# Performance work log

Hardware: AMD Instinct MI355X
Metric: run time of the kernel (lower is better)

## Reference

```python
import jax, jax.numpy as jnp
import numpy as np

N = 100000   # nodes
D = 256      # in_dim == out_dim
R = 4        # num_rel
T = 150000   # triangles per relation
H = 2        # nheads (num_rel >= 2)
DH = D // H
EPS = 1e-5


def _layernorm(x, g, b):
    m = jnp.mean(x, axis=-1, keepdims=True)
    v = jnp.mean((x - m) ** 2, axis=-1, keepdims=True)
    return (x - m) * jax.lax.rsqrt(v + EPS) * g + b


def setup_inputs() -> dict:
    key = jax.random.key(0)
    ks = jax.random.split(key, 24)
    s = 1.0 / np.sqrt(D)
    f32 = jnp.float32
    inp = {}
    inp["x"] = jax.random.normal(ks[0], (N, D), f32)
    inp["triangles"] = jax.random.randint(ks[1], (R, 3, T), 0, N)
    inp["edge_index"] = jax.random.randint(ks[2], (R, 2, 8), 0, N)
    inp["node_W"] = jax.random.normal(ks[3], (R, D, D), f32) * s
    inp["tri_W"] = jax.random.normal(ks[4], (R, D, D), f32) * s
    inp["res_W"] = jax.random.normal(ks[5], (D, D), f32) * s
    inp["gate_W"] = jax.random.normal(ks[6], (D, 2 * D), f32) * (1.0 / np.sqrt(2 * D))
    inp["gate_b"] = jnp.zeros((D,), f32)
    inp["in_W"] = jax.random.normal(ks[7], (3 * D, D), f32) * s
    inp["in_b"] = jnp.zeros((3 * D,), f32)
    inp["out_W"] = jax.random.normal(ks[8], (D, D), f32) * s
    inp["out_b"] = jnp.zeros((D,), f32)
    inp["ln1_g"] = jnp.ones((D,), f32)
    inp["ln1_b"] = jnp.zeros((D,), f32)
    inp["lin1_W"] = jax.random.normal(ks[9], (2 * D, D), f32) * s
    inp["lin1_b"] = jnp.zeros((2 * D,), f32)
    inp["lin2_W"] = jax.random.normal(ks[10], (D, 2 * D), f32) * (1.0 / np.sqrt(2 * D))
    inp["lin2_b"] = jnp.zeros((D,), f32)
    inp["ln2_g"] = jnp.ones((D,), f32)
    inp["ln2_b"] = jnp.zeros((D,), f32)
    return inp


def reference(x, triangles, edge_index, node_W, tri_W, res_W, gate_W, gate_b,
              in_W, in_b, out_W, out_b, ln1_g, ln1_b,
              lin1_W, lin1_b, lin2_W, lin2_b, ln2_g, ln2_b):
    del edge_index  # unused by the original forward
    x_res = x @ res_W.T  # [N, D]
    hs = []
    for r in range(R):  # small fixed relation count
        tri = triangles[r]                                 # [3, T]
        tri_feat = (x[tri] @ node_W[r].T).mean(axis=0)     # [T, D]
        tri_msg = tri_feat @ tri_W[r].T                    # [T, D]
        idx = tri.T.reshape(-1)                            # [3T], triangle-major
        rep = jnp.repeat(tri_msg, 3, axis=0)               # [3T, D]
        ssum = jax.ops.segment_sum(rep, idx, num_segments=N)
        cnt = jax.ops.segment_sum(jnp.ones((3 * T,), x.dtype), idx, num_segments=N)
        node_msg = ssum / jnp.maximum(cnt, 1.0)[:, None]   # scatter_mean
        u = jax.nn.elu(node_msg)                           # dropout = identity (eval)
        a = jax.nn.sigmoid(jnp.concatenate([x, u], axis=1) @ gate_W.T + gate_b)
        hs.append(jnp.tanh(u) * a + x_res * (1.0 - a))
    src = jnp.stack(hs, axis=0)                            # [R, N, D] (seq, batch, d)

    # single post-norm TransformerEncoderLayer over the relation axis
    qkv = src @ in_W.T + in_b                              # [R, N, 3D]
    q, k, v = jnp.split(qkv, 3, axis=-1)
    q = q.reshape(R, N, H, DH)
    k = k.reshape(R, N, H, DH)
    v = v.reshape(R, N, H, DH)
    scores = jnp.einsum('qnhd,knhd->nhqk', q, k) / np.sqrt(DH)
    attn = jax.nn.softmax(scores, axis=-1)
    o = jnp.einsum('nhqk,knhd->qnhd', attn, v).reshape(R, N, D)
    o = o @ out_W.T + out_b
    x1 = _layernorm(src + o, ln1_g, ln1_b)
    ff = jax.nn.gelu(x1 @ lin1_W.T + lin1_b, approximate=False) @ lin2_W.T + lin2_b
    x2 = _layernorm(x1 + ff, ln2_g, ln2_b)
    return x2.mean(axis=0)                                 # [N, D]
```

## Files before the change

kernel.cpp:

```cpp
#include <hip/hip_runtime.h>


#define NNODES 100000
#define NPAD   100096
#define DIM    256
#define NREL   4
#define NTRI   150000

typedef unsigned short ushortT;
typedef __attribute__((ext_vector_type(8)))  short   short8;
typedef __attribute__((ext_vector_type(4)))  float   floatx4;
typedef __attribute__((ext_vector_type(4)))  unsigned short ushort4v;

__device__ __forceinline__ float bf2f(ushortT u) {
    union { unsigned int i; float f; } c; c.i = ((unsigned int)u) << 16; return c.f;
}
__device__ __forceinline__ ushortT f2bf(float f) {
    union { float f; unsigned int i; } c; c.f = f;
    unsigned int x = c.i;
    x += 0x7fffu + ((x >> 16) & 1u);
    return (ushortT)(x >> 16);
}


__global__ void cvt_f32_bf16(const float* __restrict__ in, ushortT* __restrict__ out, int n4) {
    int i = blockIdx.x * blockDim.x + threadIdx.x;
    int stride = gridDim.x * blockDim.x;
    for (; i < n4; i += stride) {
        float4 v = ((const float4*)in)[i];
        ushort4v o; o.x = f2bf(v.x); o.y = f2bf(v.y); o.z = f2bf(v.z); o.w = f2bf(v.w);
        ((ushort4v*)out)[i] = o;
    }
}

__global__ void wcomb_kernel(const float* __restrict__ nodeW, const float* __restrict__ triW,
                             ushortT* __restrict__ wcomb) {
    int idx = blockIdx.x * 256 + threadIdx.x;
    int r = idx >> 16, o = (idx >> 8) & 255, k = idx & 255;
    const float* tw = triW  + ((size_t)r << 16) + o * 256;
    const float* nw = nodeW + ((size_t)r << 16) + k;
    float s = 0.f;
    #pragma unroll 8
    for (int j = 0; j < 256; ++j) s += tw[j] * nw[(size_t)j * 256];
    wcomb[idx] = f2bf(s);
}

__global__ void pack_xg(const float* __restrict__ resW, const float* __restrict__ gateW,
                        ushortT* __restrict__ o) {
    int idx = blockIdx.x * 256 + threadIdx.x;
    int r = idx >> 8, k = idx & 255;
    float v = (r < 256) ? resW[r * 256 + k] : gateW[(size_t)(r - 256) * 512 + k];
    o[idx] = f2bf(v);
}

__global__ void pack_wvo(const float* __restrict__ outW, const float* __restrict__ inW,
                         ushortT* __restrict__ o) {
    int idx = blockIdx.x * 256 + threadIdx.x;
    int r = idx >> 8, k = idx & 255;
    int orow = r & 255, d0 = (r >> 8) * 128;
    float s = 0.f;
    #pragma unroll 8
    for (int j = 0; j < 128; ++j)
        s += outW[orow * 256 + d0 + j] * inW[(size_t)(512 + d0 + j) * 256 + k];
    o[idx] = f2bf(s);
}

__global__ void calc_bvo(const float* __restrict__ outW, const float* __restrict__ in_b,
                         float* __restrict__ bvo) {
    int c = blockIdx.x * 256 + threadIdx.x;
    int orow = c & 255, d0 = (c >> 8) * 128;
    float s = 0.f;
    #pragma unroll 8
    for (int j = 0; j < 128; ++j) s += outW[orow * 256 + d0 + j] * in_b[512 + d0 + j];
    bvo[c] = s;
}


__global__ void k_count(const int* __restrict__ tri3, int* __restrict__ cnt, int n3) {
    int i = blockIdx.x * 256 + threadIdx.x;
    if (i < n3) atomicAdd(&cnt[tri3[i]], 1);
}

__global__ void k_scan1(const int* __restrict__ cnt, int* __restrict__ ptr,
                        int* __restrict__ bsum, int n) {
    __shared__ int s[256];
    int i = blockIdx.x * 256 + threadIdx.x;
    int v = (i < n) ? cnt[i] : 0;
    s[threadIdx.x] = v; __syncthreads();
    for (int off = 1; off < 256; off <<= 1) {
        int t = (threadIdx.x >= off) ? s[threadIdx.x - off] : 0;
        __syncthreads();
        s[threadIdx.x] += t;
        __syncthreads();
    }
    if (i < n) ptr[i] = s[threadIdx.x] - v;
    if (threadIdx.x == 255) bsum[blockIdx.x] = s[255];
}

__global__ void k_scan2(const int* __restrict__ bsum, int* __restrict__ bpre, int nb) {
    int lane = threadIdx.x & 63;
    int run = 0;
    for (int c = 0; c < nb; c += 64) {
        int idx = c + lane;
        int v = (idx < nb) ? bsum[idx] : 0;
        int incl = v;
        #pragma unroll
        for (int off = 1; off < 64; off <<= 1) {
            int t = __shfl_up(incl, off, 64);
            if (lane >= off) incl += t;
        }
        if (idx < nb) bpre[idx] = run + incl - v;
        run += __shfl(incl, 63, 64);
    }
}

__global__ void k_scan3(const int* __restrict__ bpre, int* __restrict__ ptr,
                        int* __restrict__ cursor, int n) {
    int i = blockIdx.x * 256 + threadIdx.x;
    if (i < n) { int p = ptr[i] + bpre[blockIdx.x]; ptr[i] = p; cursor[i] = p; }
}

__global__ void k_fill(const int* __restrict__ tri3, int* __restrict__ cursor,
                       int* __restrict__ adj, int n3, int T) {
    int i = blockIdx.x * 256 + threadIdx.x;
    if (i >= n3) return;
    int node = tri3[i];
    int t = i; if (t >= 2 * T) t -= 2 * T; else if (t >= T) t -= T;
    int pos = atomicAdd(&cursor[node], 1);
    adj[pos] = t;
}

__global__ __launch_bounds__(256)
void k_meanx(const int* __restrict__ tri, const ushortT* __restrict__ xb,
             ushortT* __restrict__ mx, int T) {
    int t = blockIdx.x * 4 + (threadIdx.x >> 6);
    if (t >= T) return;
    int lane = threadIdx.x & 63;
    int a = tri[t], b = tri[T + t], c = tri[2 * T + t];
    ushort4v va = *(const ushort4v*)(xb + (size_t)a * DIM + lane * 4);
    ushort4v vb = *(const ushort4v*)(xb + (size_t)b * DIM + lane * 4);
    ushort4v vc = *(const ushort4v*)(xb + (size_t)c * DIM + lane * 4);
    ushort4v o;
    o.x = f2bf((bf2f(va.x) + bf2f(vb.x) + bf2f(vc.x)) * (1.0f / 3.0f));
    o.y = f2bf((bf2f(va.y) + bf2f(vb.y) + bf2f(vc.y)) * (1.0f / 3.0f));
    o.z = f2bf((bf2f(va.z) + bf2f(vb.z) + bf2f(vc.z)) * (1.0f / 3.0f));
    o.w = f2bf((bf2f(va.w) + bf2f(vb.w) + bf2f(vc.w)) * (1.0f / 3.0f));
    *(ushort4v*)(mx + (size_t)t * DIM + lane * 4) = o;
}

__global__ __launch_bounds__(256)
void k_gather(const int* __restrict__ ptr, const int* __restrict__ cnt,
              const int* __restrict__ adj, const ushortT* __restrict__ mx,
              ushortT* __restrict__ accb, int n) {
    int node = blockIdx.x * 4 + (threadIdx.x >> 6);
    if (node >= n) return;
    int lane = threadIdx.x & 63;
    int st = ptr[node], c = cnt[node];
    float a0 = 0.f, a1 = 0.f, a2 = 0.f, a3 = 0.f;
    for (int j = 0; j < c; ++j) {
        int t = adj[st + j];
        ushort4v v = *(const ushort4v*)(mx + (size_t)t * DIM + lane * 4);
        a0 += bf2f(v.x); a1 += bf2f(v.y); a2 += bf2f(v.z); a3 += bf2f(v.w);
    }
    float inv = 1.0f / fmaxf((float)c, 1.0f);
    ushort4v o; o.x = f2bf(a0 * inv); o.y = f2bf(a1 * inv);
    o.z = f2bf(a2 * inv); o.w = f2bf(a3 * inv);
    *(ushort4v*)(accb + (size_t)node * DIM + lane * 4) = o;
}


#define BK 32

__device__ __forceinline__ void async_cp16(char* lds, const char* glb) {
    __builtin_amdgcn_global_load_lds((const __attribute__((address_space(1))) unsigned int*)glb,
                                     (__attribute__((address_space(3))) unsigned int*)lds,
                                     16, 0, 0);
}

enum { M_BF16 = 0, M_ELU = 1, M_GATE = 2, M_QKV = 3, M_RES = 4, M_GELU = 5 };

template <int MODE>
__global__ __launch_bounds__(256)
void gemm_bt(const ushortT* __restrict__ A, int lda, size_t aStrZ,
             const ushortT* __restrict__ W, int ldw, size_t wStrZ,
             int M, int K,
             ushortT* __restrict__ outB, int ldo, size_t oStrZ,
             const float* __restrict__ bias,
             const ushortT* __restrict__ aux1,
             const ushortT* __restrict__ aux2,
             int auxLd,
             const ushortT* __restrict__ resB,
             size_t resStrZ) {
    const size_t zi = blockIdx.z;
    A += zi * aStrZ; W += zi * wStrZ;
    if (outB) outB += zi * oStrZ;
    if (resB) resB += zi * resStrZ;

    __shared__ __align__(16) ushortT As[2][128 * BK];
    __shared__ __align__(16) ushortT Bs[2][128 * BK];
    const int tid  = threadIdx.x;
    const int wave = tid >> 6, lane = tid & 63;
    const int m0 = blockIdx.y * 128;
    const int n0 = blockIdx.x * 128;
    const int wm = (wave >> 1) * 64, wn = (wave & 1) * 64;

    floatx4 acc[4][4];
    #pragma unroll
    for (int i = 0; i < 4; ++i)
        #pragma unroll
        for (int j = 0; j < 4; ++j) acc[i][j] = (floatx4){0.f, 0.f, 0.f, 0.f};

    const int r4  = tid >> 2;
    const int b16 = (tid & 3) * 16;
    const char* Ab = (const char*)A + ((size_t)(m0 + r4) * lda) * 2 + b16;
    const char* Wb = (const char*)W + ((size_t)(n0 + r4) * ldw) * 2 + b16;

    const int kq = (lane >> 4) * 8;
    const int ra = wm + (lane & 15);
    const int rb = wn + (lane & 15);

    auto stage = [&](int buf, int k0) {
        char* Asl = (char*)As + buf * 8192 + wave * 1024;
        char* Bsl = (char*)Bs + buf * 8192 + wave * 1024;
        async_cp16(Asl,        Ab + k0 * 2);
        async_cp16(Asl + 4096, Ab + k0 * 2 + (size_t)64 * lda * 2);
        async_cp16(Bsl,        Wb + k0 * 2);
        async_cp16(Bsl + 4096, Wb + k0 * 2 + (size_t)64 * ldw * 2);
    };
    auto compute = [&](int buf) {
        short8 af[4], bfr[4];
        #pragma unroll
        for (int i = 0; i < 4; ++i) {
            af[i]  = *(const short8*)(&As[buf][(ra + i * 16) * BK + kq]);
            bfr[i] = *(const short8*)(&Bs[buf][(rb + i * 16) * BK + kq]);
        }
        #pragma unroll
        for (int mi = 0; mi < 4; ++mi)
            #pragma unroll
            for (int ni = 0; ni < 4; ++ni)
                acc[mi][ni] = __builtin_amdgcn_mfma_f32_16x16x32_bf16(af[mi], bfr[ni], acc[mi][ni], 0, 0, 0);
    };

    stage(0, 0);
    __syncthreads();
    int cur = 0;
    for (int k0 = BK; k0 < K; k0 += BK) {
        stage(cur ^ 1, k0);
        compute(cur);
        __syncthreads();
        cur ^= 1;
    }
    compute(cur);

    const int cl = lane & 15, rw = (lane >> 4) * 4;
    #pragma unroll
    for (int mi = 0; mi < 4; ++mi) {
        #pragma unroll
        for (int e = 0; e < 4; ++e) {
            const int m = m0 + wm + mi * 16 + rw + e;
            if (m >= M) continue;
            #pragma unroll
            for (int ni = 0; ni < 4; ++ni) {
                const int col = n0 + wn + ni * 16 + cl;
                float c = acc[mi][ni][e];
                if (MODE == M_BF16) {
                    outB[(size_t)m * ldo + col] = f2bf(c);
                } else if (MODE == M_ELU) {
                    c = c > 0.f ? c : (__expf(c) - 1.0f);
                    outB[(size_t)m * ldo + col] = f2bf(c);
                } else if (MODE == M_GATE) {
                    float g  = bf2f(aux1[(size_t)m * auxLd + col]);
                    float xr = bf2f(aux2[(size_t)m * auxLd + col]);
                    float uv = bf2f(A[(size_t)m * lda + col]);
                    float a  = 1.0f / (1.0f + __expf(-(c + g + bias[col])));
                    float th = 1.0f - 2.0f / (__expf(2.0f * uv) + 1.0f);
                    float h  = th * a + xr * (1.0f - a);
                    outB[(size_t)m * ldo + col] = f2bf(h);
                } else if (MODE == M_QKV) {
                    outB[(size_t)m * ldo + col] = f2bf(c + bias[col]);
                } else if (MODE == M_RES) {
                    outB[(size_t)m * ldo + col] =
                        f2bf(c + bias[col] + bf2f(resB[(size_t)m * 256 + col]));
                } else if (MODE == M_GELU) {
                    float t = c + bias[col];
                    outB[(size_t)m * ldo + col] = f2bf(0.5f * t * (1.0f + erff(t * 0.70710678118f)));
                }
            }
        }
    }
}

__global__ __launch_bounds__(256)
void attn_score(const ushortT* __restrict__ qk, size_t rstride,
                float* __restrict__ Aw, int nvalid) {
    int n = blockIdx.x * 4 + (threadIdx.x >> 6);
    if (n >= nvalid) return;
    int lane = threadIdx.x & 63;
    int head = lane >> 5, hl = lane & 31;
    int d = head * 128 + hl * 4;
    float q[NREL][4], k[NREL][4];
    #pragma unroll
    for (int r = 0; r < NREL; ++r) {
        const ushortT* base = qk + r * rstride + (size_t)n * 512;
        ushort4v qv = *(const ushort4v*)(base + d);
        ushort4v kv = *(const ushort4v*)(base + 256 + d);
        q[r][0] = bf2f(qv.x); q[r][1] = bf2f(qv.y); q[r][2] = bf2f(qv.z); q[r][3] = bf2f(qv.w);
        k[r][0] = bf2f(kv.x); k[r][1] = bf2f(kv.y); k[r][2] = bf2f(kv.z); k[r][3] = bf2f(kv.w);
    }
    float s[NREL][NREL];
    #pragma unroll
    for (int qr = 0; qr < NREL; ++qr)
        #pragma unroll
        for (int kr = 0; kr < NREL; ++kr) {
            float p = q[qr][0] * k[kr][0] + q[qr][1] * k[kr][1] +
                      q[qr][2] * k[kr][2] + q[qr][3] * k[kr][3];
            #pragma unroll
            for (int off = 1; off < 32; off <<= 1) p += __shfl_xor(p, off, 32);
            s[qr][kr] = p * 0.08838834764831845f;
        }
    if (hl < 16) {
        int qr = hl >> 2, kr = hl & 3;
        float mx = fmaxf(fmaxf(s[qr][0], s[qr][1]), fmaxf(s[qr][2], s[qr][3]));
        float e0 = __expf(s[qr][0] - mx), e1 = __expf(s[qr][1] - mx);
        float e2 = __expf(s[qr][2] - mx), e3 = __expf(s[qr][3] - mx);
        float e  = __expf(s[qr][kr] - mx);
        Aw[((size_t)n * 2 + head) * 16 + qr * 4 + kr] = e / (e0 + e1 + e2 + e3);
    }
}

__global__ __launch_bounds__(256)
void attn_combine_ln1(const ushortT* __restrict__ vo4, size_t rstride,
                      const ushortT* __restrict__ h4, size_t hstride,
                      const float* __restrict__ Aw,
                      const float* __restrict__ ob,
                      const float* __restrict__ g, const float* __restrict__ b,
                      ushortT* __restrict__ x1, size_t x1str, int nvalid) {
    int n = blockIdx.x * 4 + (threadIdx.x >> 6);
    if (n >= nvalid) return;
    int lane = threadIdx.x & 63;
    int d4 = lane * 4;
    const float* ap = Aw + (size_t)n * 32;
    float a0[NREL][NREL], a1[NREL][NREL];
    #pragma unroll
    for (int qr = 0; qr < NREL; ++qr)
        #pragma unroll
        for (int kr = 0; kr < NREL; ++kr) {
            a0[qr][kr] = ap[qr * 4 + kr];
            a1[qr][kr] = ap[16 + qr * 4 + kr];
        }
    float vl[NREL][4], vh[NREL][4];
    #pragma unroll
    for (int kr = 0; kr < NREL; ++kr) {
        const ushortT* base = vo4 + kr * rstride + (size_t)n * 512;
        ushort4v lo = *(const ushort4v*)(base + d4);
        ushort4v hi = *(const ushort4v*)(base + 256 + d4);
        vl[kr][0] = bf2f(lo.x); vl[kr][1] = bf2f(lo.y); vl[kr][2] = bf2f(lo.z); vl[kr][3] = bf2f(lo.w);
        vh[kr][0] = bf2f(hi.x); vh[kr][1] = bf2f(hi.y); vh[kr][2] = bf2f(hi.z); vh[kr][3] = bf2f(hi.w);
    }
    float bb0 = ob[d4], bb1 = ob[d4 + 1], bb2 = ob[d4 + 2], bb3 = ob[d4 + 3];
    float g0 = g[d4], g1 = g[d4 + 1], g2 = g[d4 + 2], g3 = g[d4 + 3];
    float e0 = b[d4], e1 = b[d4 + 1], e2 = b[d4 + 2], e3 = b[d4 + 3];
    #pragma unroll
    for (int qr = 0; qr < NREL; ++qr) {
        ushort4v hv = *(const ushort4v*)(h4 + qr * hstride + (size_t)n * 256 + d4);
        float z0 = bf2f(hv.x) + bb0, z1 = bf2f(hv.y) + bb1;
        float z2 = bf2f(hv.z) + bb2, z3 = bf2f(hv.w) + bb3;
        #pragma unroll
        for (int kr = 0; kr < NREL; ++kr) {
            float c0 = a0[qr][kr], c1 = a1[qr][kr];
            z0 += c0 * vl[kr][0] + c1 * vh[kr][0];
            z1 += c0 * vl[kr][1] + c1 * vh[kr][1];
            z2 += c0 * vl[kr][2] + c1 * vh[kr][2];
            z3 += c0 * vl[kr][3] + c1 * vh[kr][3];
        }
        float s = z0 + z1 + z2 + z3;
        #pragma unroll
        for (int off = 1; off < 64; off <<= 1) s += __shfl_xor(s, off, 64);
        float mean = s * (1.0f / 256.0f);
        float dx = z0 - mean, dy = z1 - mean, dz = z2 - mean, dw = z3 - mean;
        float qs = dx * dx + dy * dy + dz * dz + dw * dw;
        #pragma unroll
        for (int off = 1; off < 64; off <<= 1) qs += __shfl_xor(qs, off, 64);
        float rstd = rsqrtf(qs * (1.0f / 256.0f) + 1e-5f);
        ushort4v o;
        o.x = f2bf(dx * rstd * g0 + e0); o.y = f2bf(dy * rstd * g1 + e1);
        o.z = f2bf(dz * rstd * g2 + e2); o.w = f2bf(dw * rstd * g3 + e3);
        *(ushort4v*)(x1 + qr * x1str + (size_t)n * 256 + d4) = o;
    }
}

__global__ __launch_bounds__(256)
void ln2_out(const ushortT* __restrict__ zb, size_t zStrZ,
             const float* __restrict__ g, const float* __restrict__ b,
             float* __restrict__ outc, int n) {
    int row = blockIdx.x * 4 + (threadIdx.x >> 6);
    if (row >= n) return;
    int lane = threadIdx.x & 63, c0 = lane * 4;
    float g0 = g[c0], g1 = g[c0 + 1], g2 = g[c0 + 2], g3 = g[c0 + 3];
    float b0 = b[c0], b1 = b[c0 + 1], b2 = b[c0 + 2], b3 = b[c0 + 3];
    float o0 = 0.f, o1 = 0.f, o2 = 0.f, o3 = 0.f;
    #pragma unroll
    for (int r = 0; r < NREL; ++r) {
        ushort4v v = *(const ushort4v*)(zb + r * zStrZ + (size_t)row * 256 + c0);
        float vx = bf2f(v.x), vy = bf2f(v.y), vz = bf2f(v.z), vw = bf2f(v.w);
        float s = vx + vy + vz + vw;
        #pragma unroll
        for (int off = 1; off < 64; off <<= 1) s += __shfl_xor(s, off, 64);
        float mean = s * (1.0f / 256.0f);
        float dx = vx - mean, dy = vy - mean, dz = vz - mean, dw = vw - mean;
        float qs = dx * dx + dy * dy + dz * dz + dw * dw;
        #pragma unroll
        for (int off = 1; off < 64; off <<= 1) qs += __shfl_xor(qs, off, 64);
        float rstd = rsqrtf(qs * (1.0f / 256.0f) + 1e-5f);
        o0 += 0.25f * (dx * rstd * g0 + b0);
        o1 += 0.25f * (dy * rstd * g1 + b1);
        o2 += 0.25f * (dz * rstd * g2 + b2);
        o3 += 0.25f * (dw * rstd * g3 + b3);
    }
    float4 o; o.x = o0; o.y = o1; o.z = o2; o.w = o3;
    *(float4*)(outc + (size_t)row * 256 + c0) = o;
}


extern "C" void kernel_launch(void* const* d_in, const int* in_sizes, int n_in,
                              void* d_out, int out_size, void* d_ws, size_t ws_size,
                              hipStream_t stream) {
    const float* x      = (const float*)d_in[0];
    const int*   tri    = (const int*)d_in[1];
    const float* nodeW  = (const float*)d_in[3];
    const float* triW   = (const float*)d_in[4];
    const float* resW   = (const float*)d_in[5];
    const float* gateW  = (const float*)d_in[6];
    const float* gate_b = (const float*)d_in[7];
    const float* inW    = (const float*)d_in[8];
    const float* in_b   = (const float*)d_in[9];
    const float* outW   = (const float*)d_in[10];
    const float* out_b  = (const float*)d_in[11];
    const float* ln1g   = (const float*)d_in[12];
    const float* ln1b   = (const float*)d_in[13];
    const float* lin1W  = (const float*)d_in[14];
    const float* lin1b  = (const float*)d_in[15];
    const float* lin2W  = (const float*)d_in[16];
    const float* lin2b  = (const float*)d_in[17];
    const float* ln2g   = (const float*)d_in[18];
    const float* ln2b   = (const float*)d_in[19];
    float* out = (float*)d_out;

    char* ws = (char*)d_ws;
    size_t off = 0;
    auto alloc = [&](size_t bytes) -> char* {
        char* p = ws + off; off += (bytes + 255) & ~(size_t)255; return p;
    };
    ushortT* accAll  = (ushortT*)alloc((size_t)NREL * NPAD * 256 * 2);
    ushortT* xall_b  = (ushortT*)alloc((size_t)NPAD * 256 * 2);
    ushortT* wcomb   = (ushortT*)alloc((size_t)NREL * 65536 * 2);
    ushortT* xgW_b   = (ushortT*)alloc((size_t)131072 * 2);
    ushortT* gateW_b = (ushortT*)alloc((size_t)131072 * 2);
    ushortT* inW_b   = (ushortT*)alloc((size_t)131072 * 2);
    ushortT* wvo_b   = (ushortT*)alloc((size_t)131072 * 2);
    ushortT* lin1_bf = (ushortT*)alloc((size_t)131072 * 2);
    ushortT* lin2_bf = (ushortT*)alloc((size_t)131072 * 2);
    float*   bvo     = (float*)  alloc((size_t)512 * 4);
    size_t persist = off;
    size_t scratch = (ws_size > persist) ? (ws_size - persist) : 0;
    char* S = ws + persist;

    const size_t csrBytes = (size_t)NPAD * 4 * 3 + 4096 * 2 + (size_t)3 * NTRI * 4;
    const size_t mxBytes  = (size_t)NTRI * 256 * 2;
    if (scratch < csrBytes + mxBytes + 65536) return;
    int*     cntI   = (int*)(S);
    int*     ptrI   = (int*)(S + (size_t)NPAD * 4);
    int*     curI   = (int*)(S + (size_t)NPAD * 8);
    int*     bsum   = (int*)(S + (size_t)NPAD * 12);
    int*     bpre   = (int*)(S + (size_t)NPAD * 12 + 4096);
    int*     adj    = (int*)(S + (size_t)NPAD * 12 + 8192);
    ushortT* mxbf   = (ushortT*)(S + ((csrBytes + 255) & ~(size_t)255));

    const size_t ROWB = 9344;
    int TT = (NNODES + 127) / 128;
    int tpcMax = (int)(scratch / (ROWB * 128));
    if (tpcMax < 1) return;
    if (tpcMax > TT) tpcMax = TT;
    const int nchunks = (TT + tpcMax - 1) / tpcMax;
    const int tpc = (TT + nchunks - 1) / nchunks;
    const size_t NcPad = (size_t)tpc * 128;

    ushortT* xg   = (ushortT*)(S);
    ushortT* ubf4 = (ushortT*)(S + 1024 * NcPad);
    ushortT* h4   = (ushortT*)(S + 3072 * NcPad);
    ushortT* qk4  = (ushortT*)(S + 5120 * NcPad);
    ushortT* vo4  = qk4;
    ushortT* x1   = (ushortT*)(S);
    ushortT* ffg  = (ushortT*)(S + 2048 * NcPad);
    ushortT* zbb  = (ushortT*)(S + 6144 * NcPad);
    float*   Aw   = (float*)  (S + 9216 * NcPad);

    cvt_f32_bf16<<<2048, 256, 0, stream>>>(x, xall_b, NNODES * 64);
    cvt_f32_bf16<<<64, 256, 0, stream>>>(gateW, gateW_b, 131072 / 4);
    cvt_f32_bf16<<<64, 256, 0, stream>>>(inW,   inW_b,   131072 / 4);
    cvt_f32_bf16<<<64, 256, 0, stream>>>(lin1W, lin1_bf, 131072 / 4);
    cvt_f32_bf16<<<64, 256, 0, stream>>>(lin2W, lin2_bf, 131072 / 4);
    pack_xg<<<512, 256, 0, stream>>>(resW, gateW, xgW_b);
    pack_wvo<<<512, 256, 0, stream>>>(outW, inW, wvo_b);
    calc_bvo<<<2, 256, 0, stream>>>(outW, in_b, bvo);
    wcomb_kernel<<<1024, 256, 0, stream>>>(nodeW, triW, wcomb);

    const int NB = (NNODES + 255) / 256;
    for (int r = 0; r < NREL; ++r) {
        const int* trir = tri + (size_t)r * 3 * NTRI;
        (void)hipMemsetAsync(cntI, 0, (size_t)NPAD * 4, stream);
        k_count<<<(3 * NTRI + 255) / 256, 256, 0, stream>>>(trir, cntI, 3 * NTRI);
        k_scan1<<<NB, 256, 0, stream>>>(cntI, ptrI, bsum, NNODES);
        k_scan2<<<1, 64, 0, stream>>>(bsum, bpre, NB);
        k_scan3<<<NB, 256, 0, stream>>>(bpre, ptrI, curI, NNODES);
        k_fill<<<(3 * NTRI + 255) / 256, 256, 0, stream>>>(trir, curI, adj, 3 * NTRI, NTRI);
        k_meanx<<<(NTRI + 3) / 4, 256, 0, stream>>>(trir, xall_b, mxbf, NTRI);
        k_gather<<<(NNODES + 3) / 4, 256, 0, stream>>>(ptrI, cntI, adj, mxbf,
            accAll + (size_t)r * NPAD * 256, NNODES);
    }

    for (int ci = 0; ci < nchunks; ++ci) {
        const int rows0 = ci * tpc * 128;
        int mact = NNODES - rows0;
        if (mact <= 0) break;
        if (mact > tpc * 128) mact = tpc * 128;
        const int tiles = (mact + 127) / 128;
        const dim3 g2z(2, tiles, NREL), g4z(4, tiles, NREL);
        const int nwblk = (mact + 3) / 4;
        float* outc = out + (size_t)rows0 * 256;
        const ushortT* xbf = xall_b + (size_t)rows0 * 256;

        gemm_bt<M_BF16><<<dim3(4, tiles), 256, 0, stream>>>(xbf, 256, 0, xgW_b, 256, 0, mact, 256,
            xg, 512, 0, nullptr, nullptr, nullptr, 0, nullptr, 0);
        gemm_bt<M_ELU><<<g2z, 256, 0, stream>>>(
            accAll + (size_t)rows0 * 256, 256, (size_t)NPAD * 256,
            wcomb, 256, 65536, mact, 256,
            ubf4, 256, 256 * NcPad, nullptr, nullptr, nullptr, 0, nullptr, 0);
        gemm_bt<M_GATE><<<g2z, 256, 0, stream>>>(
            ubf4, 256, 256 * NcPad, gateW_b + 256, 512, 0, mact, 256,
            h4, 256, 256 * NcPad, gate_b, xg + 256, xg, 512, nullptr, 0);
        gemm_bt<M_QKV><<<g4z, 256, 0, stream>>>(
            h4, 256, 256 * NcPad, inW_b, 256, 0, mact, 256,
            qk4, 512, 512 * NcPad, in_b, nullptr, nullptr, 0, nullptr, 0);
        attn_score<<<nwblk, 256, 0, stream>>>(qk4, 512 * NcPad, Aw, mact);
        gemm_bt<M_QKV><<<g4z, 256, 0, stream>>>(
            h4, 256, 256 * NcPad, wvo_b, 256, 0, mact, 256,
            vo4, 512, 512 * NcPad, bvo, nullptr, nullptr, 0, nullptr, 0);
        attn_combine_ln1<<<nwblk, 256, 0, stream>>>(vo4, 512 * NcPad, h4, 256 * NcPad,
            Aw, out_b, ln1g, ln1b, x1, 256 * NcPad, mact);
        gemm_bt<M_GELU><<<g4z, 256, 0, stream>>>(x1, 256, 256 * NcPad, lin1_bf, 256, 0, mact, 256,
            ffg, 512, 512 * NcPad, lin1b, nullptr, nullptr, 0, nullptr, 0);
        gemm_bt<M_RES><<<g2z, 256, 0, stream>>>(ffg, 512, 512 * NcPad, lin2_bf, 512, 0, mact, 512,
            zbb, 256, 256 * NcPad, lin2b, nullptr, nullptr, 0, x1, 256 * NcPad);
        ln2_out<<<nwblk, 256, 0, stream>>>(zbb, 256 * NcPad, ln2g, ln2b, outc, mact);
    }
}
```

Measured before the change: 3.314 ms.

## Batch CSR build across relations, triple-buffer GEMM, cap chunk size

Builds the per-relation CSR adjacency for all four relations in one batched set of launches instead of a per-relation loop, which cuts launch count and serialization. The GEMM moves from double- to triple-buffered LDS staging, with explicit vmcnt waits and raw barriers, so global loads run two stages ahead of compute. Node chunks are capped at 120 MB, which may keep the working set in cache but adds more chunks. Costs: more LDS per block, which can lower occupancy, and extra scratch for four CSR copies.

Measured after the change: 3.441 ms. 1.04x slower.

```diff
diff --git a/kernel.cpp b/kernel.cpp
--- a/kernel.cpp
+++ b/kernel.cpp
@@ -76,13 +76,18 @@
 }
 
 
-__global__ void k_count(const int* __restrict__ tri3, int* __restrict__ cnt, int n3) {
+__global__ void k_count4(const int* __restrict__ tri, int* __restrict__ cnt4, int n3) {
+    int r = blockIdx.y;
     int i = blockIdx.x * 256 + threadIdx.x;
-    if (i < n3) atomicAdd(&cnt[tri3[i]], 1);
-}
-
-__global__ void k_scan1(const int* __restrict__ cnt, int* __restrict__ ptr,
-                        int* __restrict__ bsum, int n) {
+    if (i < n3) atomicAdd(&cnt4[r * NPAD + tri[(size_t)r * n3 + i]], 1);
+}
+
+__global__ void k_scan1(const int* __restrict__ cnt4, int* __restrict__ ptr4,
+                        int* __restrict__ bsum4, int n) {
+    int r = blockIdx.y;
+    const int* cnt = cnt4 + r * NPAD;
+    int* ptr = ptr4 + r * NPAD;
+    int* bsum = bsum4 + r * 512;
     __shared__ int s[256];
     int i = blockIdx.x * 256 + threadIdx.x;
     int v = (i < n) ? cnt[i] : 0;
@@ -97,7 +102,10 @@
     if (threadIdx.x == 255) bsum[blockIdx.x] = s[255];
 }
 
-__global__ void k_scan2(const int* __restrict__ bsum, int* __restrict__ bpre, int nb) {
+__global__ void k_scan2(const int* __restrict__ bsum4, int* __restrict__ bpre4, int nb) {
+    int r = blockIdx.x;
+    const int* bsum = bsum4 + r * 512;
+    int* bpre = bpre4 + r * 512;
     int lane = threadIdx.x & 63;
     int run = 0;
     for (int c = 0; c < nb; c += 64) {
@@ -114,20 +122,25 @@
     }
 }
 
-__global__ void k_scan3(const int* __restrict__ bpre, int* __restrict__ ptr,
-                        int* __restrict__ cursor, int n) {
+__global__ void k_scan3(const int* __restrict__ bpre4, int* __restrict__ ptr4,
+                        int* __restrict__ cur4, int n) {
+    int r = blockIdx.y;
     int i = blockIdx.x * 256 + threadIdx.x;
-    if (i < n) { int p = ptr[i] + bpre[blockIdx.x]; ptr[i] = p; cursor[i] = p; }
-}
-
-__global__ void k_fill(const int* __restrict__ tri3, int* __restrict__ cursor,
-                       int* __restrict__ adj, int n3, int T) {
+    if (i < n) {
+        int p = ptr4[r * NPAD + i] + bpre4[r * 512 + blockIdx.x];
+        ptr4[r * NPAD + i] = p; cur4[r * NPAD + i] = p;
+    }
+}
+
+__global__ void k_fill4(const int* __restrict__ tri, int* __restrict__ cur4,
+                        int* __restrict__ adj4, int n3, int T) {
+    int r = blockIdx.y;
     int i = blockIdx.x * 256 + threadIdx.x;
     if (i >= n3) return;
-    int node = tri3[i];
+    int node = tri[(size_t)r * n3 + i];
     int t = i; if (t >= 2 * T) t -= 2 * T; else if (t >= T) t -= T;
-    int pos = atomicAdd(&cursor[node], 1);
-    adj[pos] = t;
+    int pos = atomicAdd(&cur4[r * NPAD + node], 1);
+    adj4[(size_t)r * n3 + pos] = t;
 }
 
 __global__ __launch_bounds__(256)
@@ -196,8 +209,8 @@
     if (outB) outB += zi * oStrZ;
     if (resB) resB += zi * resStrZ;
 
-    __shared__ __align__(16) ushortT As[2][128 * BK];
-    __shared__ __align__(16) ushortT Bs[2][128 * BK];
+    __shared__ __align__(16) ushortT As[3][128 * BK];
+    __shared__ __align__(16) ushortT Bs[3][128 * BK];
     const int tid  = threadIdx.x;
     const int wave = tid >> 6, lane = tid & 63;
     const int m0 = blockIdx.y * 128;
@@ -241,16 +254,24 @@
                 acc[mi][ni] = __builtin_amdgcn_mfma_f32_16x16x32_bf16(af[mi], bfr[ni], acc[mi][ni], 0, 0, 0);
     };
 
+    const int NIT = K / BK;
     stage(0, 0);
-    __syncthreads();
-    int cur = 0;
-    for (int k0 = BK; k0 < K; k0 += BK) {
-        stage(cur ^ 1, k0);
-        compute(cur);
-        __syncthreads();
-        cur ^= 1;
-    }
-    compute(cur);
+    stage(1, BK);
+    asm volatile("s_waitcnt vmcnt(4)" ::: "memory");
+    __builtin_amdgcn_s_barrier();
+
+    int bufc = 0, bufs = 2;
+    for (int it = 0; it < NIT; ++it) {
+        if (it + 2 < NIT) stage(bufs, (it + 2) * BK);
+        compute(bufc);
+        if (it + 1 < NIT) {
+            if (it + 2 < NIT) asm volatile("s_waitcnt vmcnt(4)" ::: "memory");
+            else              asm volatile("s_waitcnt vmcnt(0)" ::: "memory");
+            __builtin_amdgcn_s_barrier();
+        }
+        bufc = (bufc == 2) ? 0 : bufc + 1;
+        bufs = (bufs == 2) ? 0 : bufs + 1;
+    }
 
     const int cl = lane & 15, rw = (lane >> 4) * 4;
     #pragma unroll
@@ -465,20 +486,23 @@
     size_t scratch = (ws_size > persist) ? (ws_size - persist) : 0;
     char* S = ws + persist;
 
-    const size_t csrBytes = (size_t)NPAD * 4 * 3 + 4096 * 2 + (size_t)3 * NTRI * 4;
-    const size_t mxBytes  = (size_t)NTRI * 256 * 2;
+    int*     cnt4  = (int*)(S);
+    int*     ptr4  = cnt4 + 4 * NPAD;
+    int*     cur4  = ptr4 + 4 * NPAD;
+    int*     bsum4 = cur4 + 4 * NPAD;
+    int*     bpre4 = bsum4 + 4 * 512;
+    int*     adj4  = bpre4 + 4 * 512;
+    size_t csrBytes = ((char*)(adj4 + (size_t)4 * 3 * NTRI) - S + 255) & ~(size_t)255;
+    const size_t mxBytes = (size_t)NTRI * 256 * 2;
     if (scratch < csrBytes + mxBytes + 65536) return;
-    int*     cntI   = (int*)(S);
-    int*     ptrI   = (int*)(S + (size_t)NPAD * 4);
-    int*     curI   = (int*)(S + (size_t)NPAD * 8);
-    int*     bsum   = (int*)(S + (size_t)NPAD * 12);
-    int*     bpre   = (int*)(S + (size_t)NPAD * 12 + 4096);
-    int*     adj    = (int*)(S + (size_t)NPAD * 12 + 8192);
-    ushortT* mxbf   = (ushortT*)(S + ((csrBytes + 255) & ~(size_t)255));
+    ushortT* mxbf = (ushortT*)(S + csrBytes);
 
     const size_t ROWB = 9344;
     int TT = (NNODES + 127) / 128;
-    int tpcMax = (int)(scratch / (ROWB * 128));
+    size_t budget = scratch;
+    const size_t chunkCap = (size_t)120 * 1024 * 1024;
+    if (budget > chunkCap) budget = chunkCap;
+    int tpcMax = (int)(budget / (ROWB * 128));
     if (tpcMax < 1) return;
     if (tpcMax > TT) tpcMax = TT;
     const int nchunks = (TT + tpcMax - 1) / tpcMax;
@@ -506,16 +530,19 @@
     wcomb_kernel<<<1024, 256, 0, stream>>>(nodeW, triW, wcomb);
 
     const int NB = (NNODES + 255) / 256;
+    const int N3B = (3 * NTRI + 255) / 256;
+    (void)hipMemsetAsync(cnt4, 0, (size_t)4 * NPAD * 4, stream);
+    k_count4<<<dim3(N3B, 4), 256, 0, stream>>>(tri, cnt4, 3 * NTRI);
+    k_scan1<<<dim3(NB, 4), 256, 0, stream>>>(cnt4, ptr4, bsum4, NNODES);
+    k_scan2<<<4, 64, 0, stream>>>(bsum4, bpre4, NB);
+    k_scan3<<<dim3(NB, 4), 256, 0, stream>>>(bpre4, ptr4, cur4, NNODES);
+    k_fill4<<<dim3(N3B, 4), 256, 0, stream>>>(tri, cur4, adj4, 3 * NTRI, NTRI);
     for (int r = 0; r < NREL; ++r) {
         const int* trir = tri + (size_t)r * 3 * NTRI;
-        (void)hipMemsetAsync(cntI, 0, (size_t)NPAD * 4, stream);
-        k_count<<<(3 * NTRI + 255) / 256, 256, 0, stream>>>(trir, cntI, 3 * NTRI);
-        k_scan1<<<NB, 256, 0, stream>>>(cntI, ptrI, bsum, NNODES);
-        k_scan2<<<1, 64, 0, stream>>>(bsum, bpre, NB);
-        k_scan3<<<NB, 256, 0, stream>>>(bpre, ptrI, curI, NNODES);
-        k_fill<<<(3 * NTRI + 255) / 256, 256, 0, stream>>>(trir, curI, adj, 3 * NTRI, NTRI);
         k_meanx<<<(NTRI + 3) / 4, 256, 0, stream>>>(trir, xall_b, mxbf, NTRI);
-        k_gather<<<(NNODES + 3) / 4, 256, 0, stream>>>(ptrI, cntI, adj, mxbf,
+        k_gather<<<(NNODES + 3) / 4, 256, 0, stream>>>(
+            ptr4 + (size_t)r * NPAD, cnt4 + (size_t)r * NPAD,
+            adj4 + (size_t)r * 3 * NTRI, mxbf,
             accAll + (size_t)r * NPAD * 256, NNODES);
     }
 
```
